# Performance work log

Hardware: AMD Instinct MI355X
Metric: run time of the kernel (lower is better)

## Reference

```python
import jax, jax.numpy as jnp
import numpy as np

B, N, T, F_IN = 16, 1024, 12, 1
D_MODEL, D_K, D_V, H, K = 512, 32, 32, 3, 3
C = 32  # nb_chev_filter == nb_time_filter


def _ln(x, g, b, eps=1e-5):
    mu = jnp.mean(x, -1, keepdims=True)
    var = jnp.var(x, -1, keepdims=True)
    return (x - mu) * jax.lax.rsqrt(var + eps) * g + b


def _conv(x, w, b):
    y = jax.lax.conv_general_dilated(x, w, (1, 1), 'VALID',
                                     dimension_numbers=('NCHW', 'OIHW', 'NCHW'))
    return y + b[None, :, None, None]


def setup_inputs() -> dict:
    key = jax.random.key(0)
    ks = iter(jax.random.split(key, 40))
    rn = lambda s, sc=0.02: jax.random.normal(next(ks), s, jnp.float32) * sc
    return dict(
        x=rn((B, N, F_IN, T), 1.0),
        res_att=rn((B, F_IN, H, T, T), 0.1),
        pos_embed_T=rn((T, N)),
        gamma_T=jnp.ones((N,)), beta_T=jnp.zeros((N,)),
        WQ_t=rn((N, D_K * H)), WK_t=rn((N, D_K * H)), WV_t=rn((N, D_V * H)),
        fc_t=rn((H * D_V, N)),
        pre_conv_w=rn((D_MODEL, T, 1, F_IN)), pre_conv_b=rn((D_MODEL,)),
        pos_embed_S=rn((N, D_MODEL)),
        gamma_S=jnp.ones((D_MODEL,)), beta_S=jnp.zeros((D_MODEL,)),
        WQ_s=rn((D_MODEL, D_K * K)), WK_s=rn((D_MODEL, D_K * K)),
        cheb_polys=rn((K, N, N), 0.05),
        adj_pa=(jax.random.uniform(next(ks), (N, N)) < 0.01).astype(jnp.float32),
        cheb_mask=rn((K, N, N)),
        Theta=rn((K, F_IN, C), 0.1),
        gtu3_w=rn((2 * C, C, 1, 3)), gtu3_b=rn((2 * C,)),
        gtu5_w=rn((2 * C, C, 1, 5)), gtu5_b=rn((2 * C,)),
        gtu7_w=rn((2 * C, C, 1, 7)), gtu7_b=rn((2 * C,)),
        res_conv_w=rn((C, F_IN, 1, 1)), res_conv_b=rn((C,)),
        fcmy_w=rn((3 * T - 12, T)), fcmy_b=rn((T,)),
        gamma_f=jnp.ones((C,)), beta_f=jnp.zeros((C,)),
    )


def reference(x, res_att, pos_embed_T, gamma_T, beta_T, WQ_t, WK_t, WV_t, fc_t,
              pre_conv_w, pre_conv_b, pos_embed_S, gamma_S, beta_S, WQ_s, WK_s,
              cheb_polys, adj_pa, cheb_mask, Theta,
              gtu3_w, gtu3_b, gtu5_w, gtu5_b, gtu7_w, gtu7_b,
              res_conv_w, res_conv_b, fcmy_w, fcmy_b, gamma_f, beta_f):
    B_, N_, F_, T_ = x.shape
    # ---- temporal embedding (num_of_features == 1 branch): (B,F,T,N) ----
    TEmx = _ln(jnp.transpose(x, (0, 2, 3, 1)) + pos_embed_T[None, None], gamma_T, beta_T)

    # ---- temporal MHA with residual attention bias ----
    def heads(e, W, d):
        y = e @ W  # (B,F,T,H*d)
        return jnp.transpose(y.reshape(B_, F_, T_, H, d), (0, 1, 3, 2, 4))  # (B,F,H,T,d)
    Q, Kt, V = heads(TEmx, WQ_t, D_K), heads(TEmx, WK_t, D_K), heads(TEmx, WV_t, D_V)
    re_At = jnp.einsum('bfhqd,bfhkd->bfhqk', Q, Kt) / np.sqrt(D_K) + res_att
    attn = jax.nn.softmax(re_At, axis=-1)
    ctx = jnp.einsum('bfhqk,bfhkd->bfhqd', attn, V)
    ctx = jnp.transpose(ctx, (0, 1, 3, 2, 4)).reshape(B_, F_, T_, H * D_V)
    one_n, zero_n = jnp.ones((N_,), x.dtype), jnp.zeros((N_,), x.dtype)
    TATout = _ln(ctx @ fc_t + TEmx, one_n, zero_n)  # fresh LayerNorm(d_model) -> gamma=1, beta=0

    # ---- pre_conv: Conv2d(T, d_model, kernel=(1,F)) on (B,T,N,F); take last col ----
    x_TAt = jnp.einsum('btnf,dtf->bnd', jnp.transpose(TATout, (0, 2, 3, 1)),
                       pre_conv_w[:, :, 0, :]) + pre_conv_b  # (B,N,d_model)

    # ---- spatial embedding + spatial attention scores (no softmax) ----
    SEmx = _ln(x_TAt + pos_embed_S[None], gamma_S, beta_S)  # dropout = identity (eval)
    Qs = jnp.transpose((SEmx @ WQ_s).reshape(B_, N_, K, D_K), (0, 2, 1, 3))
    Ks = jnp.transpose((SEmx @ WK_s).reshape(B_, N_, K, D_K), (0, 2, 1, 3))
    STAt = jnp.einsum('bknd,bkmd->bknm', Qs, Ks) / np.sqrt(D_K)  # (B,K,N,N)

    # ---- Chebyshev graph conv weighted by spatial attention ----
    satt = jax.nn.softmax(STAt + (adj_pa[None] * cheb_mask)[None], axis=2)
    Tka = cheb_polys[None] * satt  # (B,K,N,N)
    rhs = jnp.einsum('bkmn,bmft->bknft', Tka, x)  # T_k_with_at^T @ x over all t
    spatial_gcn = jax.nn.relu(jnp.einsum('bknft,kfo->bnot', rhs, Theta))  # (B,N,C,T)

    # ---- gated temporal convs (GTU) ----
    X = jnp.transpose(spatial_gcn, (0, 2, 1, 3))  # (B,C,N,T)
    def gtu(w, b):
        y = _conv(X, w, b)
        return jnp.tanh(y[:, :C]) * jax.nn.sigmoid(y[:, C:])
    time_conv = jnp.concatenate([gtu(gtu3_w, gtu3_b), gtu(gtu5_w, gtu5_b),
                                 gtu(gtu7_w, gtu7_b)], axis=-1)  # (B,C,N,3T-12)
    time_conv = time_conv @ fcmy_w + fcmy_b  # (B,C,N,T)
    tco = jax.nn.relu(time_conv)  # num_of_features == 1 branch

    # ---- residual 1x1 conv + final LayerNorm over channel dim ----
    x_res = _conv(jnp.transpose(x, (0, 2, 1, 3)), res_conv_w, res_conv_b)  # (B,C,N,T)
    out = _ln(jnp.transpose(jax.nn.relu(x_res + tco), (0, 3, 2, 1)), gamma_f, beta_f)
    out = jnp.transpose(out, (0, 2, 3, 1))  # (B,N,C,T)
    return out, re_At
```

## Files before the change

kernel.cpp:

```cpp
#include <hip/hip_runtime.h>
#include <hip/hip_bf16.h>
#include <math.h>

#define B_ 16
#define N_ 1024
#define T_ 12
#define DM_ 512
#define H_ 3
#define K_ 3
#define C_ 32
#define RSQRT_DK 0.17677669529663687f

typedef __attribute__((ext_vector_type(8))) short bf16x8;
typedef __attribute__((ext_vector_type(4))) float f32x4;

__device__ __forceinline__ ushort f2bf(float f) {
  uint u = __float_as_uint(f);
  return (ushort)((u + 0x7FFF + ((u >> 16) & 1)) >> 16);
}

__global__ void k1_temporal_ln(const float* __restrict__ x, const float* __restrict__ posT,
                               const float* __restrict__ gT, const float* __restrict__ bT,
                               float* __restrict__ TEmx) {
  int row = blockIdx.x;
  int b = row / T_, t = row - b * T_;
  __shared__ float red[256], red2[256];
  float v[4]; float s = 0.f, s2 = 0.f;
  for (int i = 0; i < 4; ++i) {
    int n = threadIdx.x + (i << 8);
    float val = x[(b * N_ + n) * T_ + t] + posT[t * N_ + n];
    v[i] = val; s += val; s2 += val * val;
  }
  red[threadIdx.x] = s; red2[threadIdx.x] = s2;
  __syncthreads();
  for (int off = 128; off > 0; off >>= 1) {
    if (threadIdx.x < off) { red[threadIdx.x] += red[threadIdx.x + off]; red2[threadIdx.x] += red2[threadIdx.x + off]; }
    __syncthreads();
  }
  float mu = red[0] * (1.f / N_);
  float rs = rsqrtf(red2[0] * (1.f / N_) - mu * mu + 1e-5f);
  for (int i = 0; i < 4; ++i) {
    int n = threadIdx.x + (i << 8);
    TEmx[row * N_ + n] = (v[i] - mu) * rs * gT[n] + bT[n];
  }
}

__global__ __launch_bounds__(256) void k2_qkv(const float* __restrict__ TEmx,
                       const float* __restrict__ WQ, const float* __restrict__ WK,
                       const float* __restrict__ WV, float* __restrict__ part) {
  int kc = blockIdx.x, row = blockIdx.y;
  __shared__ float e[256];
  int tid = threadIdx.x;
  e[tid] = TEmx[row * N_ + kc * 256 + tid];
  __syncthreads();
  for (int col = tid; col < 288; col += 256) {
    int which = col / 96, j = col - which * 96;
    const float* W = (which == 0) ? WQ : ((which == 1) ? WK : WV);
    const float* Wp = W + (size_t)(kc * 256) * 96 + j;
    float acc = 0.f;
    #pragma unroll 8
    for (int n = 0; n < 256; ++n) acc += e[n] * Wp[n * 96];
    part[(row * 4 + kc) * 288 + col] = acc;
  }
}

__global__ void k3a_attn(const float* __restrict__ part, const float* __restrict__ res_att,
                         float* __restrict__ reAt_out, float* __restrict__ ctx) {
  int b = blockIdx.x;
  __shared__ float q_l[T_ * 288];
  __shared__ float s_l[H_ * T_ * T_];
  for (int i = threadIdx.x; i < T_ * 288; i += 256) {
    int t = i / 288, col = i - t * 288;
    const float* pr = &part[(size_t)((b * T_ + t) * 4) * 288 + col];
    q_l[i] = pr[0] + pr[288] + pr[576] + pr[864];
  }
  __syncthreads();
  for (int idx = threadIdx.x; idx < H_ * T_ * T_; idx += 256) {
    int h = idx / 144, r = idx - h * 144, qi = r / 12, ki = r - qi * 12;
    float acc = 0.f;
    #pragma unroll
    for (int d = 0; d < 32; ++d)
      acc += q_l[qi * 288 + h * 32 + d] * q_l[ki * 288 + 96 + h * 32 + d];
    float sv = acc * RSQRT_DK + res_att[(b * H_ + h) * 144 + qi * 12 + ki];
    s_l[idx] = sv;
    reAt_out[(b * H_ + h) * 144 + qi * 12 + ki] = sv;
  }
  __syncthreads();
  if (threadIdx.x < 36) {
    int h = threadIdx.x / 12, qi = threadIdx.x - h * 12;
    float mx = -1e30f;
    for (int ki = 0; ki < 12; ++ki) mx = fmaxf(mx, s_l[h * 144 + qi * 12 + ki]);
    float sum = 0.f;
    for (int ki = 0; ki < 12; ++ki) { float p = __expf(s_l[h * 144 + qi * 12 + ki] - mx); s_l[h * 144 + qi * 12 + ki] = p; sum += p; }
    float inv = 1.f / sum;
    for (int ki = 0; ki < 12; ++ki) s_l[h * 144 + qi * 12 + ki] *= inv;
  }
  __syncthreads();
  for (int idx = threadIdx.x; idx < T_ * 96; idx += 256) {
    int qi = idx / 96, hd = idx - qi * 96, h = hd >> 5, d = hd & 31;
    float acc = 0.f;
    for (int ki = 0; ki < 12; ++ki)
      acc += s_l[h * 144 + qi * 12 + ki] * q_l[ki * 288 + 192 + h * 32 + d];
    ctx[(b * T_ + qi) * 96 + hd] = acc;
  }
}

__global__ __launch_bounds__(1024) void k3b_tat(const float* __restrict__ ctx,
                        const float* __restrict__ fc_t,
                        const float* __restrict__ TEmx, float* __restrict__ TAT) {
  int row = blockIdx.x;
  __shared__ float c_l[96];
  __shared__ float red[16], red2[16];
  int tid = threadIdx.x;
  if (tid < 96) c_l[tid] = ctx[row * 96 + tid];
  __syncthreads();
  float acc = TEmx[row * N_ + tid];
  #pragma unroll 12
  for (int j = 0; j < 96; ++j) acc = fmaf(c_l[j], fc_t[j * N_ + tid], acc);
  float s = acc, s2 = acc * acc;
  #pragma unroll
  for (int off = 32; off > 0; off >>= 1) {
    s  += __shfl_xor(s, off);
    s2 += __shfl_xor(s2, off);
  }
  int w = tid >> 6;
  if ((tid & 63) == 0) { red[w] = s; red2[w] = s2; }
  __syncthreads();
  float ts = 0.f, ts2 = 0.f;
  #pragma unroll
  for (int i = 0; i < 16; ++i) { ts += red[i]; ts2 += red2[i]; }
  float mu = ts * (1.f / N_);
  float rs = rsqrtf(ts2 * (1.f / N_) - mu * mu + 1e-5f);
  TAT[row * N_ + tid] = (acc - mu) * rs;
}

__global__ void k4_preconv_ln(const float* __restrict__ TAT, const float* __restrict__ pcw,
                              const float* __restrict__ pcb, const float* __restrict__ posS,
                              const float* __restrict__ gS, const float* __restrict__ bS,
                              float* __restrict__ SEmx) {
  int bn = blockIdx.x; int b = bn >> 10, n = bn & 1023;
  __shared__ float tc[12];
  __shared__ float red[256], red2[256];
  if (threadIdx.x < 12) tc[threadIdx.x] = TAT[(b * T_ + threadIdx.x) * N_ + n];
  __syncthreads();
  float v[2]; float s = 0.f, s2 = 0.f;
  for (int i = 0; i < 2; ++i) {
    int d = threadIdx.x + (i << 8);
    float acc = pcb[d];
    #pragma unroll
    for (int t = 0; t < 12; ++t) acc += tc[t] * pcw[d * 12 + t];
    acc += posS[n * DM_ + d];
    v[i] = acc; s += acc; s2 += acc * acc;
  }
  red[threadIdx.x] = s; red2[threadIdx.x] = s2;
  __syncthreads();
  for (int off = 128; off > 0; off >>= 1) {
    if (threadIdx.x < off) { red[threadIdx.x] += red[threadIdx.x + off]; red2[threadIdx.x] += red2[threadIdx.x + off]; }
    __syncthreads();
  }
  float mu = red[0] * (1.f / DM_);
  float rs = rsqrtf(red2[0] * (1.f / DM_) - mu * mu + 1e-5f);
  for (int i = 0; i < 2; ++i) {
    int d = threadIdx.x + (i << 8);
    SEmx[bn * DM_ + d] = (v[i] - mu) * rs * gS[d] + bS[d];
  }
}

__global__ void k5_pre(const float* __restrict__ WQs, const float* __restrict__ WKs,
                       ushort* __restrict__ wpre) {
  int idx = blockIdx.x * 256 + threadIdx.x;
  int k = idx / 192, col = idx - k * 192;
  float v = (col < 96) ? WQs[k * 96 + col] : WKs[k * 96 + (col - 96)];
  wpre[col * 512 + k] = f2bf(v);
}

__global__ __launch_bounds__(256) void k5_qks(const float* __restrict__ SEmx,
                                              const ushort* __restrict__ wpre,
                                              __hip_bfloat16* __restrict__ Qs,
                                              __hip_bfloat16* __restrict__ Ks) {
  int b = blockIdx.y, n0 = blockIdx.x * 32;
  __shared__ __align__(16) ushort SE_h[32 * 520];
  int tid = threadIdx.x;
  for (int idx = tid; idx < 4096; idx += 256) {
    int r = idx >> 7, cq = idx & 127;
    float4 v = *(const float4*)&SEmx[((size_t)((b << 10) + n0 + r)) * DM_ + cq * 4];
    uint lo = (uint)f2bf(v.x) | ((uint)f2bf(v.y) << 16);
    uint hi = (uint)f2bf(v.z) | ((uint)f2bf(v.w) << 16);
    *(uint2*)&SE_h[r * 520 + cq * 4] = make_uint2(lo, hi);
  }
  __syncthreads();

  int w = tid >> 6, lane = tid & 63, quad = lane >> 4, c16 = lane & 15;
  f32x4 acc[3][2];
  #pragma unroll
  for (int mi = 0; mi < 3; ++mi)
    #pragma unroll
    for (int nt = 0; nt < 2; ++nt) acc[mi][nt] = (f32x4){0.f, 0.f, 0.f, 0.f};

  for (int ks = 0; ks < 16; ++ks) {
    bf16x8 Bf0 = *(const bf16x8*)&SE_h[(0 * 16 + c16) * 520 + ks * 32 + quad * 8];
    bf16x8 Bf1 = *(const bf16x8*)&SE_h[(1 * 16 + c16) * 520 + ks * 32 + quad * 8];
    #pragma unroll
    for (int mi = 0; mi < 3; ++mi) {
      int m = (w * 3 + mi) * 16 + c16;
      bf16x8 Af = *(const bf16x8*)&wpre[m * 512 + ks * 32 + quad * 8];
      acc[mi][0] = __builtin_amdgcn_mfma_f32_16x16x32_bf16(Af, Bf0, acc[mi][0], 0, 0, 0);
      acc[mi][1] = __builtin_amdgcn_mfma_f32_16x16x32_bf16(Af, Bf1, acc[mi][1], 0, 0, 0);
    }
  }
  #pragma unroll
  for (int mi = 0; mi < 3; ++mi) {
    int mb = (w * 3 + mi) * 16;
    #pragma unroll
    for (int nt = 0; nt < 2; ++nt) {
      int node = n0 + nt * 16 + c16;
      #pragma unroll
      for (int r = 0; r < 4; ++r) {
        int m = mb + quad * 4 + r;
        int j = (m < 96) ? m : m - 96;
        int kk = j >> 5, dd = j & 31;
        __hip_bfloat16* o = (m < 96) ? Qs : Ks;
        o[(((b * K_ + kk) * N_) + node) * 32 + dd] = __float2bfloat16(acc[mi][nt][r]);
      }
    }
  }
}

__global__ void k6_pre(const float* __restrict__ adj, const float* __restrict__ mask,
                       const float* __restrict__ cheb, uint* __restrict__ pk) {
  int idx = blockIdx.x * 256 + threadIdx.x;
  int mn = idx & (N_ * N_ - 1);
  uint lo = f2bf(adj[mn] * mask[idx]);
  uint hi = f2bf(cheb[idx]);
  pk[idx] = lo | (hi << 16);
}

__global__ __launch_bounds__(256) void k6_spatial(
    const __hip_bfloat16* __restrict__ Qs, const __hip_bfloat16* __restrict__ Ks,
    const uint* __restrict__ pk, const float* __restrict__ x,
    float* __restrict__ rhs) {
  const int b  = blockIdx.x;
  const int k  = blockIdx.y;
  const int n0 = blockIdx.z * 32;
  const ushort* Qb = (const ushort*)(Qs + (size_t)((b * K_ + k) * N_) * 32);
  const ushort* Kb = (const ushort*)(Ks + (size_t)((b * K_ + k) * N_) * 32);
  const uint* pkk = pk + (size_t)k * (N_ * N_);
  const float* xb = x + b * N_ * T_;

  __shared__ float wmu[4][32], well[4][32];
  __shared__ float wacc[4][32][12];

  const int tid  = threadIdx.x;
  const int w    = tid >> 6, lane = tid & 63;
  const int quad = lane >> 4, c16 = lane & 15;

  bf16x8 bfr0 = *(const bf16x8*)(Kb + (size_t)(n0 + c16) * 32 + quad * 8);
  bf16x8 bfr1 = *(const bf16x8*)(Kb + (size_t)(n0 + 16 + c16) * 32 + quad * 8);

  float mu0 = -1e30f, mu1 = -1e30f, el0 = 0.f, el1 = 0.f;
  float acc0[12], acc1[12];
  #pragma unroll
  for (int t = 0; t < 12; ++t) { acc0[t] = 0.f; acc1[t] = 0.f; }

  for (int s = 0; s < 16; ++s) {
    const int m0 = s * 64 + w * 16;
    bf16x8 af = *(const bf16x8*)(Qb + (size_t)(m0 + c16) * 32 + quad * 8);
    f32x4 z = {0.f, 0.f, 0.f, 0.f};
    f32x4 sc0 = __builtin_amdgcn_mfma_f32_16x16x32_bf16(af, bfr0, z, 0, 0, 0);
    f32x4 sc1 = __builtin_amdgcn_mfma_f32_16x16x32_bf16(af, bfr1, z, 0, 0, 0);

    const int mrow = m0 + quad * 4;
    float sv0[4], sv1[4], ch0[4], ch1[4];
    #pragma unroll
    for (int r = 0; r < 4; ++r) {
      uint p2 = pkk[(size_t)(mrow + r) * N_ + n0 + c16];
      uint q2 = pkk[(size_t)(mrow + r) * N_ + n0 + 16 + c16];
      sv0[r] = sc0[r] * RSQRT_DK + __uint_as_float(p2 << 16);
      ch0[r] = __uint_as_float(p2 & 0xFFFF0000u);
      sv1[r] = sc1[r] * RSQRT_DK + __uint_as_float(q2 << 16);
      ch1[r] = __uint_as_float(q2 & 0xFFFF0000u);
    }
    float cm0 = fmaxf(fmaxf(sv0[0], sv0[1]), fmaxf(sv0[2], sv0[3]));
    float cm1 = fmaxf(fmaxf(sv1[0], sv1[1]), fmaxf(sv1[2], sv1[3]));
    cm0 = fmaxf(cm0, __shfl_xor(cm0, 16)); cm0 = fmaxf(cm0, __shfl_xor(cm0, 32));
    cm1 = fmaxf(cm1, __shfl_xor(cm1, 16)); cm1 = fmaxf(cm1, __shfl_xor(cm1, 32));
    float nm0 = fmaxf(mu0, cm0), nm1 = fmaxf(mu1, cm1);
    float f0 = __expf(mu0 - nm0), f1 = __expf(mu1 - nm1);
    mu0 = nm0; mu1 = nm1;
    el0 *= f0; el1 *= f1;
    #pragma unroll
    for (int t = 0; t < 12; ++t) { acc0[t] *= f0; acc1[t] *= f1; }

    float p0[4], p1[4];
    #pragma unroll
    for (int r = 0; r < 4; ++r) {
      p0[r] = __expf(sv0[r] - mu0); el0 += p0[r]; p0[r] *= ch0[r];
      p1[r] = __expf(sv1[r] - mu1); el1 += p1[r]; p1[r] *= ch1[r];
    }
    #pragma unroll
    for (int r = 0; r < 4; ++r) {
      const float4* xr = (const float4*)(xb + (size_t)(mrow + r) * 12);
      float4 xA = xr[0], xB = xr[1], xC = xr[2];
      float xv[12] = {xA.x, xA.y, xA.z, xA.w, xB.x, xB.y, xB.z, xB.w,
                      xC.x, xC.y, xC.z, xC.w};
      float px0 = p0[r], px1 = p1[r];
      #pragma unroll
      for (int t = 0; t < 12; ++t) {
        acc0[t] = fmaf(px0, xv[t], acc0[t]);
        acc1[t] = fmaf(px1, xv[t], acc1[t]);
      }
    }
  }

  #pragma unroll
  for (int off = 16; off <= 32; off <<= 1) {
    el0 += __shfl_xor(el0, off);
    el1 += __shfl_xor(el1, off);
    #pragma unroll
    for (int t = 0; t < 12; ++t) {
      acc0[t] += __shfl_xor(acc0[t], off);
      acc1[t] += __shfl_xor(acc1[t], off);
    }
  }
  if (quad == 0) {
    wmu[w][c16] = mu0; well[w][c16] = el0;
    #pragma unroll
    for (int t = 0; t < 12; ++t) wacc[w][c16][t] = acc0[t];
  } else if (quad == 1) {
    wmu[w][16 + c16] = mu1; well[w][16 + c16] = el1;
    #pragma unroll
    for (int t = 0; t < 12; ++t) wacc[w][16 + c16][t] = acc1[t];
  }
  __syncthreads();
  if (tid < 384) {
    int n = tid / 12, t = tid - n * 12;
    float m0v = wmu[0][n], m1v = wmu[1][n], m2v = wmu[2][n], m3v = wmu[3][n];
    float gm = fmaxf(fmaxf(m0v, m1v), fmaxf(m2v, m3v));
    float e0 = __expf(m0v - gm), e1 = __expf(m1v - gm);
    float e2 = __expf(m2v - gm), e3 = __expf(m3v - gm);
    float den = well[0][n] * e0 + well[1][n] * e1 + well[2][n] * e2 + well[3][n] * e3;
    float num = wacc[0][n][t] * e0 + wacc[1][n][t] * e1 +
                wacc[2][n][t] * e2 + wacc[3][n][t] * e3;
    rhs[((size_t)(b * K_ + k) * N_ + n0 + n) * 12 + t] = num / den;
  }
}

template<int KS, int JV, int JB>
__device__ __forceinline__ void conv_mfma(const ushort* X_th, const ushort* wl_h,
                                          ushort* tc_h, const float* bias0,
                                          int mp, int ntg, int quad, int c16) {
  f32x4 accA[3], accB[3];
  #pragma unroll
  for (int i = 0; i < 3; ++i) { accA[i] = (f32x4){0.f,0.f,0.f,0.f}; accB[i] = (f32x4){0.f,0.f,0.f,0.f}; }
  #pragma unroll
  for (int dt = 0; dt < KS; ++dt) {
    bf16x8 A0 = *(const bf16x8*)&wl_h[dt * 2560 + (mp * 16 + c16) * 40 + quad * 8];
    bf16x8 A1 = *(const bf16x8*)&wl_h[dt * 2560 + ((mp + 2) * 16 + c16) * 40 + quad * 8];
    #pragma unroll
    for (int i = 0; i < 3; ++i) {
      int nt = ntg * 3 + i;
      int j = nt >> 1, sh = nt & 1;
      bf16x8 Bf = *(const bf16x8*)&X_th[(sh * 16 + c16) * 584 + (j + dt) * 32 + quad * 8];
      accA[i] = __builtin_amdgcn_mfma_f32_16x16x32_bf16(A0, Bf, accA[i], 0, 0, 0);
      accB[i] = __builtin_amdgcn_mfma_f32_16x16x32_bf16(A1, Bf, accB[i], 0, 0, 0);
    }
  }
  #pragma unroll
  for (int i = 0; i < 3; ++i) {
    int nt = ntg * 3 + i, j = nt >> 1, sh = nt & 1;
    if (j < JV) {
      int s = sh * 16 + c16;
      int sx = (s & 15) << 1;
      #pragma unroll
      for (int r = 0; r < 4; ++r) {
        int cc = mp * 16 + quad * 4 + r;
        float a = accA[i][r] + bias0[cc];
        float g = accB[i][r] + bias0[cc + 32];
        float e2a = __expf(2.f * a);
        float th = 1.f - 2.f / (e2a + 1.f);
        float sg = 1.f / (1.f + __expf(-g));
        tc_h[((s * 32 + cc) * 32 + (JB + j)) ^ sx] = f2bf(th * sg);
      }
    }
  }
}

__global__ __launch_bounds__(1024) void k8_fused(
                       const float* __restrict__ rhs, const float* __restrict__ Theta,
                       const float* __restrict__ x, const float* __restrict__ rw,
                       const float* __restrict__ rb,
                       const float* __restrict__ w3, const float* __restrict__ b3,
                       const float* __restrict__ w5, const float* __restrict__ b5,
                       const float* __restrict__ w7, const float* __restrict__ b7,
                       const float* __restrict__ fw, const float* __restrict__ fb,
                       const float* __restrict__ gf, const float* __restrict__ bf,
                       float* __restrict__ out) {
  int bn0 = blockIdx.x * 32;
  int b = bn0 >> 10, n0 = bn0 & 1023;

  __shared__ __align__(16) char uR[73216];
  ushort* X_th = (ushort*)uR;
  ushort* wl_h = (ushort*)(uR + 37376);
  float*  v_l  = (float*)uR;
  __shared__ __align__(16) ushort tc_h[1024 * 32];
  __shared__ float rhs_l[32 * 36];
  __shared__ float Th_l[96];
  __shared__ float xr_l[32 * 12];
  __shared__ float fw_l[288];
  __shared__ float fb_l[12];
  __shared__ float bias_l[3][64];
  __shared__ float rw_l[32], rb_l[32], gf_l[32], bf_l[32];
  __shared__ float stm[384], str[384];

  int tid = threadIdx.x;
  int w = tid >> 6, lane = tid & 63, quad = lane >> 4, c16 = lane & 15;
  int mp = w & 1, ntg = w >> 1;
  int c = (tid >> 3) & 31;
  int site = (tid & 7) | ((tid >> 8) << 3);

  for (int idx = tid; idx < 1152; idx += 1024) {
    int s = idx / 36, r = idx - s * 36, k = r / 12, t = r - k * 12;
    rhs_l[idx] = rhs[((size_t)(b * 3 + k) * N_ + n0 + s) * 12 + t];
  }
  if (tid < 384) xr_l[tid] = x[(size_t)(b * N_ + n0) * 12 + tid];
  if (tid < 96) Th_l[tid] = Theta[tid];
  if (tid < 288) fw_l[tid] = fw[tid];
  if (tid < 12) fb_l[tid] = fb[tid];
  if (tid < 64) { bias_l[0][tid] = b3[tid]; bias_l[1][tid] = b5[tid]; bias_l[2][tid] = b7[tid]; }
  if (tid >= 64 && tid < 96)  rw_l[tid - 64] = rw[tid - 64];
  if (tid >= 96 && tid < 128) rb_l[tid - 96] = rb[tid - 96];
  if (tid >= 128 && tid < 160) gf_l[tid - 128] = gf[tid - 128];
  if (tid >= 160 && tid < 192) bf_l[tid - 160] = bf[tid - 160];
  for (int idx = tid; idx < 64 * 32 * 3; idx += 1024) {
    int co = idx / 96, r2 = idx - co * 96, ic = r2 / 3, dt = r2 - ic * 3;
    wl_h[dt * 2560 + co * 40 + ic] = f2bf(w3[idx]);
  }
  __syncthreads();

  {
    float th0 = Th_l[c], th1 = Th_l[32 + c], th2 = Th_l[64 + c];
    const float* rs_ = &rhs_l[site * 36];
    ushort* xo = &X_th[site * 584 + c];
    #pragma unroll
    for (int t = 0; t < 12; ++t) {
      float a = rs_[t] * th0 + rs_[12 + t] * th1 + rs_[24 + t] * th2;
      xo[t * 32] = f2bf(fmaxf(a, 0.f));
    }
  }
  for (int idx = tid; idx < 32 * 6 * 32; idx += 1024) {
    int s = idx / 192, r2 = idx - s * 192, tt = r2 >> 5, ic = r2 & 31;
    X_th[s * 584 + (12 + tt) * 32 + ic] = 0;
  }
  __syncthreads();

  conv_mfma<3, 10, 0>(X_th, wl_h, tc_h, &bias_l[0][0], mp, ntg, quad, c16);
  __syncthreads();
  for (int idx = tid; idx < 64 * 32 * 5; idx += 1024) {
    int co = idx / 160, r2 = idx - co * 160, ic = r2 / 5, dt = r2 - ic * 5;
    wl_h[dt * 2560 + co * 40 + ic] = f2bf(w5[idx]);
  }
  __syncthreads();
  conv_mfma<5, 8, 10>(X_th, wl_h, tc_h, &bias_l[1][0], mp, ntg, quad, c16);
  __syncthreads();
  for (int idx = tid; idx < 64 * 32 * 7; idx += 1024) {
    int co = idx / 224, r2 = idx - co * 224, ic = r2 / 7, dt = r2 - ic * 7;
    wl_h[dt * 2560 + co * 40 + ic] = f2bf(w7[idx]);
  }
  __syncthreads();
  conv_mfma<7, 6, 18>(X_th, wl_h, tc_h, &bias_l[2][0], mp, ntg, quad, c16);
  __syncthreads();

  float tcv[24];
  {
    int rb2 = (site * 32 + c) * 32;
    int sx = (site & 15) << 1;
    #pragma unroll
    for (int j = 0; j < 24; ++j)
      tcv[j] = __uint_as_float(((uint)tc_h[(rb2 + j) ^ sx]) << 16);
  }
  float o[12];
  #pragma unroll
  for (int t = 0; t < 12; ++t) o[t] = fb_l[t];
  #pragma unroll
  for (int j = 0; j < 24; ++j) {
    const float4* fp = (const float4*)&fw_l[j * 12];
    float4 f0 = fp[0], f1 = fp[1], f2 = fp[2];
    float fr[12] = {f0.x, f0.y, f0.z, f0.w, f1.x, f1.y, f1.z, f1.w, f2.x, f2.y, f2.z, f2.w};
    #pragma unroll
    for (int t = 0; t < 12; ++t) o[t] = fmaf(tcv[j], fr[t], o[t]);
  }

  float v[12];
  {
    float rwc = rw_l[c], rbc = rb_l[c];
    const float* xs = &xr_l[site * 12];
    float* vo = &v_l[site * 391 + c * 12];
    #pragma unroll
    for (int t = 0; t < 12; ++t) {
      float xres = xs[t] * rwc + rbc;
      v[t] = fmaxf(xres + fmaxf(o[t], 0.f), 0.f);
      vo[t] = v[t];
    }
  }
  __syncthreads();
  if (tid < 384) {
    int s = tid / 12, t = tid - s * 12;
    float sm = 0.f, s2 = 0.f;
    #pragma unroll 8
    for (int cc = 0; cc < 32; ++cc) {
      float u = v_l[s * 391 + cc * 12 + t];
      sm += u; s2 += u * u;
    }
    float m = sm * (1.f / 32.f);
    stm[tid] = m;
    str[tid] = rsqrtf(s2 * (1.f / 32.f) - m * m + 1e-5f);
  }
  __syncthreads();
  {
    float gfc = gf_l[c], bfc = bf_l[c];
    const float* sm_ = &stm[site * 12];
    const float* sr_ = &str[site * 12];
    float q[12];
    #pragma unroll
    for (int t = 0; t < 12; ++t) q[t] = (v[t] - sm_[t]) * sr_[t] * gfc + bfc;
    float* op = &out[(size_t)(bn0 + site) * 384 + c * 12];
    ((float4*)op)[0] = make_float4(q[0], q[1], q[2], q[3]);
    ((float4*)op)[1] = make_float4(q[4], q[5], q[6], q[7]);
    ((float4*)op)[2] = make_float4(q[8], q[9], q[10], q[11]);
  }
}

extern "C" void kernel_launch(void* const* d_in, const int* in_sizes, int n_in,
                              void* d_out, int out_size, void* d_ws, size_t ws_size,
                              hipStream_t stream) {
  const float* x       = (const float*)d_in[0];
  const float* res_att = (const float*)d_in[1];
  const float* posT    = (const float*)d_in[2];
  const float* gT      = (const float*)d_in[3];
  const float* bT      = (const float*)d_in[4];
  const float* WQt     = (const float*)d_in[5];
  const float* WKt     = (const float*)d_in[6];
  const float* WVt     = (const float*)d_in[7];
  const float* fct     = (const float*)d_in[8];
  const float* pcw     = (const float*)d_in[9];
  const float* pcb     = (const float*)d_in[10];
  const float* posS    = (const float*)d_in[11];
  const float* gS      = (const float*)d_in[12];
  const float* bS      = (const float*)d_in[13];
  const float* WQs     = (const float*)d_in[14];
  const float* WKs     = (const float*)d_in[15];
  const float* cheb    = (const float*)d_in[16];
  const float* adj     = (const float*)d_in[17];
  const float* mask    = (const float*)d_in[18];
  const float* Theta   = (const float*)d_in[19];
  const float* w3      = (const float*)d_in[20];
  const float* b3      = (const float*)d_in[21];
  const float* w5      = (const float*)d_in[22];
  const float* b5      = (const float*)d_in[23];
  const float* w7      = (const float*)d_in[24];
  const float* b7      = (const float*)d_in[25];
  const float* rw      = (const float*)d_in[26];
  const float* rb      = (const float*)d_in[27];
  const float* fw      = (const float*)d_in[28];
  const float* fb      = (const float*)d_in[29];
  const float* gf      = (const float*)d_in[30];
  const float* bf      = (const float*)d_in[31];

  float* ws = (float*)d_ws;
  float* TEmx = ws;
  float* qkv  = TEmx + 196608;
  float* ctx  = qkv + 55296;
  float* TAT  = ctx + 18432;
  float* SEmx = TAT + 196608;
  float* Qsf  = SEmx + 8388608;
  float* Ksf  = Qsf + 1572864;
  float* rhs  = Ksf + 1572864;
  ushort* wpre = (ushort*)(rhs + 589824);
  float* part = SEmx;

  __hip_bfloat16* Qh = (__hip_bfloat16*)Qsf;
  __hip_bfloat16* Kh = (__hip_bfloat16*)Ksf;
  uint* pk = (uint*)SEmx;

  float* out  = (float*)d_out;
  float* reAt = out + 6291456;

  k5_pre<<<(DM_ * 192) / 256, 256, 0, stream>>>(WQs, WKs, wpre);
  k1_temporal_ln<<<B_ * T_, 256, 0, stream>>>(x, posT, gT, bT, TEmx);
  k2_qkv<<<dim3(4, B_ * T_), 256, 0, stream>>>(TEmx, WQt, WKt, WVt, part);
  k3a_attn<<<B_, 256, 0, stream>>>(part, res_att, reAt, ctx);
  k3b_tat<<<B_ * T_, 1024, 0, stream>>>(ctx, fct, TEmx, TAT);
  k4_preconv_ln<<<B_ * N_, 256, 0, stream>>>(TAT, pcw, pcb, posS, gS, bS, SEmx);
  k5_qks<<<dim3(N_ / 32, B_), 256, 0, stream>>>(SEmx, wpre, Qh, Kh);
  k6_pre<<<(K_ * N_ * N_) / 256, 256, 0, stream>>>(adj, mask, cheb, pk);
  k6_spatial<<<dim3(B_, K_, N_ / 32), 256, 0, stream>>>(Qh, Kh, pk, x, rhs);
  k8_fused<<<B_ * N_ / 32, 1024, 0, stream>>>(rhs, Theta, x, rw, rb,
                                              w3, b3, w5, b5, w7, b7, fw, fb, gf, bf, out);
}
```

Baseline: 351.3 us.

## Shrink fused GTU kernel LDS with per-phase fcmy accumulation and swizzled layouts

Restructures the fused GTU/output kernel to cut shared memory. The fcmy projection now accumulates into registers right after each conv phase, so only a small per-phase tc buffer is kept instead of the full 24-column one. The weight and activation tiles use XOR-swizzled layouts to avoid bank conflicts, MFMA tiles are distributed per wave with only the valid outputs computed, and the final LayerNorm statistics come from wave shuffles instead of a large staging array. rhs and x are read straight from global memory rather than staged. The aim is lower LDS use and better occupancy, at the cost of extra barriers and fcmy work interleaved between phases.

```diff
diff --git a/kernel.cpp b/kernel.cpp
--- a/kernel.cpp
+++ b/kernel.cpp
@@ -17,6 +17,9 @@
 __device__ __forceinline__ ushort f2bf(float f) {
   uint u = __float_as_uint(f);
   return (ushort)((u + 0x7FFF + ((u >> 16) & 1)) >> 16);
+}
+__device__ __forceinline__ float bf2f(ushort h) {
+  return __uint_as_float(((uint)h) << 16);
 }
 
 __global__ void k1_temporal_ln(const float* __restrict__ x, const float* __restrict__ posT,
@@ -345,47 +348,42 @@
   }
 }
 
-template<int KS, int JV, int JB>
-__device__ __forceinline__ void conv_mfma(const ushort* X_th, const ushort* wl_h,
-                                          ushort* tc_h, const float* bias0,
-                                          int mp, int ntg, int quad, int c16) {
-  f32x4 accA[3], accB[3];
-  #pragma unroll
-  for (int i = 0; i < 3; ++i) { accA[i] = (f32x4){0.f,0.f,0.f,0.f}; accB[i] = (f32x4){0.f,0.f,0.f,0.f}; }
-  #pragma unroll
-  for (int dt = 0; dt < KS; ++dt) {
-    bf16x8 A0 = *(const bf16x8*)&wl_h[dt * 2560 + (mp * 16 + c16) * 40 + quad * 8];
-    bf16x8 A1 = *(const bf16x8*)&wl_h[dt * 2560 + ((mp + 2) * 16 + c16) * 40 + quad * 8];
-    #pragma unroll
-    for (int i = 0; i < 3; ++i) {
-      int nt = ntg * 3 + i;
-      int j = nt >> 1, sh = nt & 1;
-      bf16x8 Bf = *(const bf16x8*)&X_th[(sh * 16 + c16) * 584 + (j + dt) * 32 + quad * 8];
-      accA[i] = __builtin_amdgcn_mfma_f32_16x16x32_bf16(A0, Bf, accA[i], 0, 0, 0);
-      accB[i] = __builtin_amdgcn_mfma_f32_16x16x32_bf16(A1, Bf, accB[i], 0, 0, 0);
-    }
-  }
-  #pragma unroll
-  for (int i = 0; i < 3; ++i) {
-    int nt = ntg * 3 + i, j = nt >> 1, sh = nt & 1;
-    if (j < JV) {
-      int s = sh * 16 + c16;
-      int sx = (s & 15) << 1;
-      #pragma unroll
-      for (int r = 0; r < 4; ++r) {
-        int cc = mp * 16 + quad * 4 + r;
-        float a = accA[i][r] + bias0[cc];
-        float g = accB[i][r] + bias0[cc + 32];
-        float e2a = __expf(2.f * a);
-        float th = 1.f - 2.f / (e2a + 1.f);
-        float sg = 1.f / (1.f + __expf(-g));
-        tc_h[((s * 32 + cc) * 32 + (JB + j)) ^ sx] = f2bf(th * sg);
-      }
-    }
-  }
-}
-
-__global__ __launch_bounds__(1024) void k8_fused(
+template<int KS, int JV>
+__device__ __forceinline__ void conv_phase(const ushort* Xh, const ushort* wl,
+                                           ushort* tc8, ushort* ov, const float* bias,
+                                           int w, int quad, int c16) {
+  for (int tix = w; tix < 4 * JV; tix += 16) {
+    int mp = tix & 1, sh = (tix >> 1) & 1, j = tix >> 2;
+    f32x4 aA = (f32x4){0.f, 0.f, 0.f, 0.f};
+    f32x4 aB = (f32x4){0.f, 0.f, 0.f, 0.f};
+    #pragma unroll
+    for (int dt = 0; dt < KS; ++dt) {
+      int ua = (dt * 256 + (mp * 16 + c16) * 4 + quad) ^ (c16 & 7);
+      bf16x8 A0 = *(const bf16x8*)&wl[ua << 3];
+      bf16x8 A1 = *(const bf16x8*)&wl[(ua + 128) << 3];
+      int ub = ((sh * 16 + c16) * 48 + (j + dt) * 4 + quad) ^ (c16 & 7);
+      bf16x8 Bf = *(const bf16x8*)&Xh[ub << 3];
+      aA = __builtin_amdgcn_mfma_f32_16x16x32_bf16(A0, Bf, aA, 0, 0, 0);
+      aB = __builtin_amdgcn_mfma_f32_16x16x32_bf16(A1, Bf, aB, 0, 0, 0);
+    }
+    int s = sh * 16 + c16;
+    int sx = (s & 15) << 1;
+    #pragma unroll
+    for (int r = 0; r < 4; ++r) {
+      int cc = mp * 16 + quad * 4 + r;
+      float a = aA[r] + bias[cc];
+      float g = aB[r] + bias[cc + 32];
+      float e2a = __expf(2.f * a);
+      float th = 1.f - 2.f / (e2a + 1.f);
+      float sg = 1.f / (1.f + __expf(-g));
+      ushort hv = f2bf(th * sg);
+      if (JV <= 8 || j < 8) tc8[(((s * 32 + cc) << 3) | j) ^ sx] = hv;
+      else                  ov[(((s * 32 + cc) << 1) | (j - 8)) ^ sx] = hv;
+    }
+  }
+}
+
+__global__ __launch_bounds__(1024, 8) void k8_fused(
                        const float* __restrict__ rhs, const float* __restrict__ Theta,
                        const float* __restrict__ x, const float* __restrict__ rw,
                        const float* __restrict__ rb,
@@ -398,131 +396,168 @@
   int bn0 = blockIdx.x * 32;
   int b = bn0 >> 10, n0 = bn0 & 1023;
 
-  __shared__ __align__(16) char uR[73216];
-  ushort* X_th = (ushort*)uR;
-  ushort* wl_h = (ushort*)(uR + 37376);
-  float*  v_l  = (float*)uR;
-  __shared__ __align__(16) ushort tc_h[1024 * 32];
-  __shared__ float rhs_l[32 * 36];
-  __shared__ float Th_l[96];
-  __shared__ float xr_l[32 * 12];
+  __shared__ __align__(16) char P[73728];
+  ushort* Xh  = (ushort*)P;
+  ushort* wl  = (ushort*)(P + 24576);
+  ushort* tc8 = (ushort*)(P + 53248);
+  ushort* ov  = (ushort*)(P + 69632);
+  float*  part = (float*)P;
+  float*  stm  = (float*)(P + 13824);
+  float*  str  = (float*)(P + 15360);
   __shared__ float fw_l[288];
   __shared__ float fb_l[12];
   __shared__ float bias_l[3][64];
   __shared__ float rw_l[32], rb_l[32], gf_l[32], bf_l[32];
-  __shared__ float stm[384], str[384];
 
   int tid = threadIdx.x;
   int w = tid >> 6, lane = tid & 63, quad = lane >> 4, c16 = lane & 15;
-  int mp = w & 1, ntg = w >> 1;
   int c = (tid >> 3) & 31;
   int site = (tid & 7) | ((tid >> 8) << 3);
 
-  for (int idx = tid; idx < 1152; idx += 1024) {
-    int s = idx / 36, r = idx - s * 36, k = r / 12, t = r - k * 12;
-    rhs_l[idx] = rhs[((size_t)(b * 3 + k) * N_ + n0 + s) * 12 + t];
-  }
-  if (tid < 384) xr_l[tid] = x[(size_t)(b * N_ + n0) * 12 + tid];
-  if (tid < 96) Th_l[tid] = Theta[tid];
   if (tid < 288) fw_l[tid] = fw[tid];
   if (tid < 12) fb_l[tid] = fb[tid];
-  if (tid < 64) { bias_l[0][tid] = b3[tid]; bias_l[1][tid] = b5[tid]; bias_l[2][tid] = b7[tid]; }
-  if (tid >= 64 && tid < 96)  rw_l[tid - 64] = rw[tid - 64];
-  if (tid >= 96 && tid < 128) rb_l[tid - 96] = rb[tid - 96];
-  if (tid >= 128 && tid < 160) gf_l[tid - 128] = gf[tid - 128];
-  if (tid >= 160 && tid < 192) bf_l[tid - 160] = bf[tid - 160];
-  for (int idx = tid; idx < 64 * 32 * 3; idx += 1024) {
-    int co = idx / 96, r2 = idx - co * 96, ic = r2 / 3, dt = r2 - ic * 3;
-    wl_h[dt * 2560 + co * 40 + ic] = f2bf(w3[idx]);
-  }
-  __syncthreads();
-
+  if (tid >= 320 && tid < 384) { int i2 = tid - 320; bias_l[0][i2] = b3[i2]; bias_l[1][i2] = b5[i2]; bias_l[2][i2] = b7[i2]; }
+  if (tid >= 384 && tid < 416) rw_l[tid - 384] = rw[tid - 384];
+  if (tid >= 416 && tid < 448) rb_l[tid - 416] = rb[tid - 416];
+  if (tid >= 448 && tid < 480) gf_l[tid - 448] = gf[tid - 448];
+  if (tid >= 480 && tid < 512) bf_l[tid - 480] = bf[tid - 480];
   {
-    float th0 = Th_l[c], th1 = Th_l[32 + c], th2 = Th_l[64 + c];
-    const float* rs_ = &rhs_l[site * 36];
-    ushort* xo = &X_th[site * 584 + c];
+    float th0 = Theta[c], th1 = Theta[32 + c], th2 = Theta[64 + c];
+    const float* r0 = &rhs[((size_t)(b * 3 + 0) * N_ + n0 + site) * 12];
+    const float* r1 = &rhs[((size_t)(b * 3 + 1) * N_ + n0 + site) * 12];
+    const float* r2 = &rhs[((size_t)(b * 3 + 2) * N_ + n0 + site) * 12];
     #pragma unroll
     for (int t = 0; t < 12; ++t) {
-      float a = rs_[t] * th0 + rs_[12 + t] * th1 + rs_[24 + t] * th2;
-      xo[t * 32] = f2bf(fmaxf(a, 0.f));
-    }
-  }
-  for (int idx = tid; idx < 32 * 6 * 32; idx += 1024) {
-    int s = idx / 192, r2 = idx - s * 192, tt = r2 >> 5, ic = r2 & 31;
-    X_th[s * 584 + (12 + tt) * 32 + ic] = 0;
-  }
-  __syncthreads();
-
-  conv_mfma<3, 10, 0>(X_th, wl_h, tc_h, &bias_l[0][0], mp, ntg, quad, c16);
-  __syncthreads();
-  for (int idx = tid; idx < 64 * 32 * 5; idx += 1024) {
-    int co = idx / 160, r2 = idx - co * 160, ic = r2 / 5, dt = r2 - ic * 5;
-    wl_h[dt * 2560 + co * 40 + ic] = f2bf(w5[idx]);
-  }
-  __syncthreads();
-  conv_mfma<5, 8, 10>(X_th, wl_h, tc_h, &bias_l[1][0], mp, ntg, quad, c16);
-  __syncthreads();
-  for (int idx = tid; idx < 64 * 32 * 7; idx += 1024) {
-    int co = idx / 224, r2 = idx - co * 224, ic = r2 / 7, dt = r2 - ic * 7;
-    wl_h[dt * 2560 + co * 40 + ic] = f2bf(w7[idx]);
-  }
-  __syncthreads();
-  conv_mfma<7, 6, 18>(X_th, wl_h, tc_h, &bias_l[2][0], mp, ntg, quad, c16);
-  __syncthreads();
-
-  float tcv[24];
-  {
-    int rb2 = (site * 32 + c) * 32;
-    int sx = (site & 15) << 1;
-    #pragma unroll
-    for (int j = 0; j < 24; ++j)
-      tcv[j] = __uint_as_float(((uint)tc_h[(rb2 + j) ^ sx]) << 16);
-  }
+      float a = r0[t] * th0 + r1[t] * th1 + r2[t] * th2;
+      int u = (site * 48 + t * 4 + (c >> 3)) ^ (site & 7);
+      Xh[(u << 3) | (c & 7)] = f2bf(fmaxf(a, 0.f));
+    }
+  }
+  for (int ds = tid; ds < 3 * 2048; ds += 1024) {
+    int dt = ds >> 11, r2 = ds & 2047, co = r2 >> 5, ic = r2 & 31;
+    int u = (ds >> 3) ^ (co & 7);
+    wl[(u << 3) | (ds & 7)] = f2bf(w3[(co * 32 + ic) * 3 + dt]);
+  }
+  __syncthreads();
+
+  conv_phase<3, 10>(Xh, wl, tc8, ov, &bias_l[0][0], w, quad, c16);
+  __syncthreads();
+
   float o[12];
   #pragma unroll
   for (int t = 0; t < 12; ++t) o[t] = fb_l[t];
-  #pragma unroll
-  for (int j = 0; j < 24; ++j) {
-    const float4* fp = (const float4*)&fw_l[j * 12];
-    float4 f0 = fp[0], f1 = fp[1], f2 = fp[2];
-    float fr[12] = {f0.x, f0.y, f0.z, f0.w, f1.x, f1.y, f1.z, f1.w, f2.x, f2.y, f2.z, f2.w};
-    #pragma unroll
-    for (int t = 0; t < 12; ++t) o[t] = fmaf(tcv[j], fr[t], o[t]);
-  }
-
-  float v[12];
+  {
+    int base = (site * 32 + c) << 3;
+    int sx = (site & 15) << 1;
+    for (int j = 0; j < 8; ++j) {
+      float tv = bf2f(tc8[(base | j) ^ sx]);
+      const float* fr = &fw_l[j * 12];
+      #pragma unroll
+      for (int t = 0; t < 12; ++t) o[t] = fmaf(tv, fr[t], o[t]);
+    }
+    int base2 = (site * 32 + c) << 1;
+    for (int j2 = 0; j2 < 2; ++j2) {
+      float tv = bf2f(ov[(base2 | j2) ^ sx]);
+      const float* fr = &fw_l[(8 + j2) * 12];
+      #pragma unroll
+      for (int t = 0; t < 12; ++t) o[t] = fmaf(tv, fr[t], o[t]);
+    }
+  }
+  for (int ds = tid; ds < 5 * 2048; ds += 1024) {
+    int dt = ds >> 11, r2 = ds & 2047, co = r2 >> 5, ic = r2 & 31;
+    int u = (ds >> 3) ^ (co & 7);
+    wl[(u << 3) | (ds & 7)] = f2bf(w5[(co * 32 + ic) * 5 + dt]);
+  }
+  __syncthreads();
+
+  conv_phase<5, 8>(Xh, wl, tc8, ov, &bias_l[1][0], w, quad, c16);
+  __syncthreads();
+
+  {
+    int base = (site * 32 + c) << 3;
+    int sx = (site & 15) << 1;
+    for (int j = 0; j < 8; ++j) {
+      float tv = bf2f(tc8[(base | j) ^ sx]);
+      const float* fr = &fw_l[(10 + j) * 12];
+      #pragma unroll
+      for (int t = 0; t < 12; ++t) o[t] = fmaf(tv, fr[t], o[t]);
+    }
+  }
+  for (int ds = tid; ds < 7 * 2048; ds += 1024) {
+    int dt = ds >> 11, r2 = ds & 2047, co = r2 >> 5, ic = r2 & 31;
+    int u = (ds >> 3) ^ (co & 7);
+    wl[(u << 3) | (ds & 7)] = f2bf(w7[(co * 32 + ic) * 7 + dt]);
+  }
+  __syncthreads();
+
+  conv_phase<7, 6>(Xh, wl, tc8, ov, &bias_l[2][0], w, quad, c16);
+  __syncthreads();
+
+  {
+    int base = (site * 32 + c) << 3;
+    int sx = (site & 15) << 1;
+    for (int j = 0; j < 6; ++j) {
+      float tv = bf2f(tc8[(base | j) ^ sx]);
+      const float* fr = &fw_l[(18 + j) * 12];
+      #pragma unroll
+      for (int t = 0; t < 12; ++t) o[t] = fmaf(tv, fr[t], o[t]);
+    }
+  }
+  float vv[12];
   {
     float rwc = rw_l[c], rbc = rb_l[c];
-    const float* xs = &xr_l[site * 12];
-    float* vo = &v_l[site * 391 + c * 12];
+    const float4* xg = (const float4*)&x[((size_t)(b * N_ + n0 + site)) * 12];
+    float4 xA = xg[0], xB = xg[1], xC = xg[2];
+    float xv[12] = {xA.x, xA.y, xA.z, xA.w, xB.x, xB.y, xB.z, xB.w,
+                    xC.x, xC.y, xC.z, xC.w};
     #pragma unroll
     for (int t = 0; t < 12; ++t) {
-      float xres = xs[t] * rwc + rbc;
-      v[t] = fmaxf(xres + fmaxf(o[t], 0.f), 0.f);
-      vo[t] = v[t];
-    }
-  }
-  __syncthreads();
+      float xres = xv[t] * rwc + rbc;
+      vv[t] = fmaxf(xres + fmaxf(o[t], 0.f), 0.f);
+    }
+  }
+  {
+    float ps[12], pq[12];
+    #pragma unroll
+    for (int t = 0; t < 12; ++t) { ps[t] = vv[t]; pq[t] = vv[t] * vv[t]; }
+    #pragma unroll
+    for (int off = 8; off <= 32; off <<= 1) {
+      #pragma unroll
+      for (int t = 0; t < 12; ++t) {
+        ps[t] += __shfl_xor(ps[t], off);
+        pq[t] += __shfl_xor(pq[t], off);
+      }
+    }
+    if (lane < 8) {
+      float* pp = &part[(w * 8 + lane) * 24];
+      #pragma unroll
+      for (int t = 0; t < 12; ++t) { pp[t] = ps[t]; pp[12 + t] = pq[t]; }
+    }
+  }
+  __syncthreads();
+
   if (tid < 384) {
-    int s = tid / 12, t = tid - s * 12;
-    float sm = 0.f, s2 = 0.f;
-    #pragma unroll 8
-    for (int cc = 0; cc < 32; ++cc) {
-      float u = v_l[s * 391 + cc * 12 + t];
-      sm += u; s2 += u * u;
+    int s2 = tid / 12, t2 = tid - s2 * 12;
+    int g = s2 >> 3, sl = s2 & 7;
+    float sm = 0.f, sq = 0.f;
+    #pragma unroll
+    for (int q = 0; q < 4; ++q) {
+      const float* pp = &part[((g * 4 + q) * 8 + sl) * 24];
+      sm += pp[t2]; sq += pp[12 + t2];
     }
     float m = sm * (1.f / 32.f);
     stm[tid] = m;
-    str[tid] = rsqrtf(s2 * (1.f / 32.f) - m * m + 1e-5f);
-  }
-  __syncthreads();
+    str[tid] = rsqrtf(sq * (1.f / 32.f) - m * m + 1e-5f);
+  }
+  __syncthreads();
+
   {
     float gfc = gf_l[c], bfc = bf_l[c];
     const float* sm_ = &stm[site * 12];
     const float* sr_ = &str[site * 12];
     float q[12];
     #pragma unroll
-    for (int t = 0; t < 12; ++t) q[t] = (v[t] - sm_[t]) * sr_[t] * gfc + bfc;
+    for (int t = 0; t < 12; ++t) q[t] = (vv[t] - sm_[t]) * sr_[t] * gfc + bfc;
     float* op = &out[(size_t)(bn0 + site) * 384 + c * 12];
     ((float4*)op)[0] = make_float4(q[0], q[1], q[2], q[3]);
     ((float4*)op)[1] = make_float4(q[4], q[5], q[6], q[7]);
```

After: 584.4 us. +66.4%, slower.
